# Performance work log

Measured on AMD Instinct MI355X. Metric: run time of the kernel, lower is better.

Reference implementation:

```python
import jax, jax.numpy as jnp
import numpy as np

N_NODES = 50000
N_EDGES = 800000
D_FEAT = 96
DIM_H = 128
N_CLASSES = 10


def setup_inputs() -> dict:
    key = jax.random.key(0)
    k = jax.random.split(key, 6)
    x = jax.random.normal(k[0], (N_NODES, D_FEAT), dtype=jnp.float32)
    edge_index = jax.random.randint(k[1], (2, N_EDGES), 0, N_NODES, dtype=jnp.int64)
    # Rank1Linear(dim_h): W = outer(a1, b1), a1: (in,), b1: (out,)
    a1 = jax.random.normal(k[2], (D_FEAT,), dtype=jnp.float32) / np.sqrt(D_FEAT)
    b1 = jax.random.normal(k[3], (DIM_H,), dtype=jnp.float32)
    # Rank1Linear(num_classes)
    a2 = jax.random.normal(k[4], (DIM_H,), dtype=jnp.float32) / np.sqrt(DIM_H)
    b2 = jax.random.normal(k[5], (N_CLASSES,), dtype=jnp.float32)
    return {"x": x, "edge_index": edge_index, "a1": a1, "b1": b1, "a2": a2, "b2": b2}


def reference(x, edge_index, a1, b1, a2, b2):
    src = edge_index[0]
    dst = edge_index[1]
    # adj @ x without materializing NxN: gather source features, scatter-add to dest
    agg = jax.ops.segment_sum(x[src], dst, num_segments=N_NODES)  # [N, d_feat]
    # GraphConv: rank-1 linear + ReLU. (adj @ x) @ (a1 b1^T) == ((adj@x) @ a1) outer b1
    h1 = jax.nn.relu((agg @ a1)[:, None] * b1[None, :])  # [N, dim_h]
    # sum pooling over nodes -> graph embedding [1, dim_h]; dropout is identity in eval
    hG = jnp.sum(h1, axis=0, keepdims=True)
    # final rank-1 linear to classes
    return (hG @ a2)[:, None] * b2[None, :]  # [1, num_classes]
```

## Files before the change

### kernel.cpp

```cpp
#include <hip/hip_runtime.h>

constexpr int N_NODES   = 50000;
constexpr int N_EDGES   = 800000;
constexpr int D_FEAT    = 96;
constexpr int DIM_H     = 128;
constexpr int N_CLASSES = 10;

constexpr int SHIFT  = 8;
constexpr int BNODES = 1 << SHIFT;
constexpr int NB     = (N_NODES + BNODES - 1) >> SHIFT;
constexpr int NBLK1  = 256;
constexpr int EPB    = N_EDGES / NBLK1;
constexpr int PREFW  = NB + 1;

static_assert(N_NODES <= (1 << 16), "16-bit id packing requires N_NODES <= 65536");
static_assert(N_EDGES % NBLK1 == 0, "exact edge split");
static_assert(D_FEAT % 8 == 0, "8-lane row dot needs D_FEAT % 8 == 0");

__device__ inline int wave_iscan(int v, int lane) {
#pragma unroll
    for (int off = 1; off < 64; off <<= 1) {
        int n = __shfl_up(v, off);
        if (lane >= off) v += n;
    }
    return v;
}

__device__ inline float wave_rsum(float v) {
#pragma unroll
    for (int off = 32; off > 0; off >>= 1) v += __shfl_down(v, off);
    return v;
}

__global__ __launch_bounds__(1024) void k_prep(
    const float* __restrict__ x, const float* __restrict__ a1,
    const int* __restrict__ src, const int* __restrict__ dst,
    float* __restrict__ y, unsigned* __restrict__ pairs,
    int* __restrict__ prefg, int* __restrict__ ticket)
{
    __shared__ unsigned stage[EPB];
    __shared__ int hist[NB], run[NB], excl[PREFW];
    __shared__ int wsum[16];
    const int tid  = threadIdx.x;
    const int lane = tid & 63, wid = tid >> 6;
    const int blk  = blockIdx.x;

    if (blk == 0 && tid == 0)
        __hip_atomic_store(ticket, 0, __ATOMIC_RELAXED, __HIP_MEMORY_SCOPE_AGENT);

    {
        const float4* av = reinterpret_cast<const float4*>(a1);
        const int sub = tid & 7;
        const float4 a0 = av[sub * 3 + 0];
        const float4 a1v = av[sub * 3 + 1];
        const float4 a2v = av[sub * 3 + 2];
        const int g0 = (blk * 1024 + tid) >> 3;
        for (int r = g0; r < N_NODES; r += (NBLK1 * 1024) / 8) {
            const float4* row =
                reinterpret_cast<const float4*>(x + (size_t)r * D_FEAT) + sub * 3;
            float4 v0 = row[0], v1 = row[1], v2 = row[2];
            float s = v0.x * a0.x + v0.y * a0.y + v0.z * a0.z + v0.w * a0.w
                    + v1.x * a1v.x + v1.y * a1v.y + v1.z * a1v.z + v1.w * a1v.w
                    + v2.x * a2v.x + v2.y * a2v.y + v2.z * a2v.z + v2.w * a2v.w;
            s += __shfl_xor(s, 1);
            s += __shfl_xor(s, 2);
            s += __shfl_xor(s, 4);
            if (sub == 0) y[r] = s;
        }
    }

    for (int t = tid; t < NB; t += 1024) hist[t] = 0;
    __syncthreads();
    const int e0 = blk * EPB;
    for (int j = tid; j < EPB; j += 1024)
        atomicAdd(&hist[((unsigned)dst[e0 + j]) >> SHIFT], 1);
    __syncthreads();

    int v   = (tid < NB) ? hist[tid] : 0;
    int inc = wave_iscan(v, lane);
    if (lane == 63) wsum[wid] = inc;
    __syncthreads();
    int woff = 0;
#pragma unroll
    for (int w = 0; w < 16; ++w) if (w < wid) woff += wsum[w];
    if (tid < NB) { int e = inc - v + woff; excl[tid] = e; run[tid] = e; }
    if (tid == 0) {
        int t = 0;
#pragma unroll
        for (int w = 0; w < 16; ++w) t += wsum[w];
        excl[NB] = t;
    }
    __syncthreads();
    if (tid < PREFW) prefg[blk * PREFW + tid] = excl[tid];

    for (int j = tid; j < EPB; j += 1024) {
        int d = dst[e0 + j];
        int s = src[e0 + j];
        int pos = atomicAdd(&run[((unsigned)d) >> SHIFT], 1);
        stage[pos] = ((unsigned)s << 16) | (unsigned)d;
    }
    __syncthreads();

    for (int j = tid; j < EPB; j += 1024)
        pairs[(size_t)blk * EPB + j] = stage[j];
}

__global__ __launch_bounds__(512) void k_accum_final(
    const unsigned* __restrict__ pairs, const int* __restrict__ prefg,
    const float* __restrict__ y, const float* __restrict__ b1,
    const float* __restrict__ a2, const float* __restrict__ b2,
    float* __restrict__ PMpart, int* __restrict__ ticket,
    float* __restrict__ out)
{
    __shared__ float acc[BNODES];
    __shared__ int   soff[NBLK1], scnt[NBLK1];
    __shared__ float redp[8], redm[8], redcp[8], redcn[8];
    __shared__ int   islast;
    __shared__ float tval;
    const int b    = blockIdx.x;
    const int tid  = threadIdx.x;
    const int lane = tid & 63, wid = tid >> 6;

    if (tid < BNODES) acc[tid] = 0.f;
    if (tid < NBLK1) {
        int st = prefg[tid * PREFW + b];
        soff[tid] = st;
        scnt[tid] = prefg[tid * PREFW + b + 1] - st;
    }
    __syncthreads();

    {
        const int seg = tid >> 1, h = tid & 1;
        const int n = scnt[seg];
        const unsigned* p0 = pairs + (size_t)seg * EPB + soff[seg];
        for (int j = h; j < n; j += 2) {
            unsigned p = p0[j];
            atomicAdd(&acc[p & (BNODES - 1)], y[p >> 16]);
        }
    }
    __syncthreads();

    float pp = 0.f, mm = 0.f;
    if (tid < BNODES) {
        int g = (b << SHIFT) + tid;
        if (g < N_NODES) {
            float v = acc[tid];
            pp = fmaxf(v, 0.f);
            mm = fminf(v, 0.f);
        }
    }
    pp = wave_rsum(pp);
    mm = wave_rsum(mm);
    if (lane == 0) { redp[wid] = pp; redm[wid] = mm; }
    __syncthreads();
    if (tid == 0) {
        float tp = 0.f, tm = 0.f;
#pragma unroll
        for (int w = 0; w < 8; ++w) { tp += redp[w]; tm += redm[w]; }
        __hip_atomic_store(&PMpart[2 * b],     tp, __ATOMIC_RELAXED, __HIP_MEMORY_SCOPE_AGENT);
        __hip_atomic_store(&PMpart[2 * b + 1], tm, __ATOMIC_RELAXED, __HIP_MEMORY_SCOPE_AGENT);
        int t = __hip_atomic_fetch_add(ticket, 1, __ATOMIC_ACQ_REL, __HIP_MEMORY_SCOPE_AGENT);
        islast = (t == NB - 1);
    }
    __syncthreads();

    if (islast) {
        float P = 0.f, M = 0.f, cp = 0.f, cn = 0.f;
        if (tid < NB) {
            P = __hip_atomic_load(&PMpart[2 * tid],     __ATOMIC_RELAXED, __HIP_MEMORY_SCOPE_AGENT);
            M = __hip_atomic_load(&PMpart[2 * tid + 1], __ATOMIC_RELAXED, __HIP_MEMORY_SCOPE_AGENT);
        }
        if (tid < DIM_H) {
            float bv = b1[tid], pr = a2[tid] * bv;
            cp = (bv > 0.f) ? pr : 0.f;
            cn = (bv < 0.f) ? pr : 0.f;
        }
        P  = wave_rsum(P);
        M  = wave_rsum(M);
        cp = wave_rsum(cp);
        cn = wave_rsum(cn);
        __syncthreads();
        if (lane == 0) { redp[wid] = P; redm[wid] = M; redcp[wid] = cp; redcn[wid] = cn; }
        __syncthreads();
        if (tid == 0) {
            float sP = 0.f, sM = 0.f, sCP = 0.f, sCN = 0.f;
#pragma unroll
            for (int w = 0; w < 8; ++w) {
                sP += redp[w]; sM += redm[w]; sCP += redcp[w]; sCN += redcn[w];
            }
            tval = sP * sCP + sM * sCN;
        }
        __syncthreads();
        if (tid < N_CLASSES) out[tid] = tval * b2[tid];
    }
}

__global__ void fb_node_dot(const float* __restrict__ x, const float* __restrict__ a1,
                            float* __restrict__ y) {
    int i = blockIdx.x * blockDim.x + threadIdx.x;
    if (i >= N_NODES) return;
    const float4* row = reinterpret_cast<const float4*>(x + (size_t)i * D_FEAT);
    const float4* av  = reinterpret_cast<const float4*>(a1);
    float acc = 0.f;
#pragma unroll
    for (int k = 0; k < D_FEAT / 4; ++k) {
        float4 v = row[k], a = av[k];
        acc += v.x * a.x + v.y * a.y + v.z * a.z + v.w * a.w;
    }
    y[i] = acc;
}

__global__ void fb_scatter(const int* __restrict__ src, const int* __restrict__ dst,
                           const float* __restrict__ y, float* __restrict__ s) {
    int e = blockIdx.x * blockDim.x + threadIdx.x;
    if (e >= N_EDGES) return;
    atomicAdd(&s[dst[e]], y[src[e]]);
}

__global__ void fb_reduce(const float* __restrict__ s, float* __restrict__ PM) {
    float p = 0.f, m = 0.f;
    for (int i = blockIdx.x * blockDim.x + threadIdx.x; i < N_NODES;
         i += gridDim.x * blockDim.x) {
        float v = s[i];
        p += fmaxf(v, 0.f);
        m += fminf(v, 0.f);
    }
    p = wave_rsum(p);
    m = wave_rsum(m);
    __shared__ float lp[4], lm[4];
    int wid = threadIdx.x >> 6, lane = threadIdx.x & 63;
    if (lane == 0) { lp[wid] = p; lm[wid] = m; }
    __syncthreads();
    if (threadIdx.x == 0) {
        float tp = 0.f, tm = 0.f;
        for (int w = 0; w < (int)(blockDim.x >> 6); ++w) { tp += lp[w]; tm += lm[w]; }
        atomicAdd(&PM[0], tp);
        atomicAdd(&PM[1], tm);
    }
}

__global__ void fb_final(const float* __restrict__ b1, const float* __restrict__ a2,
                         const float* __restrict__ b2, const float* __restrict__ PM,
                         float* __restrict__ out) {
    int t = threadIdx.x;
    float bv = b1[t], prod = a2[t] * bv;
    float cp = (bv > 0.f) ? prod : 0.f;
    float cn = (bv < 0.f) ? prod : 0.f;
    cp = wave_rsum(cp);
    cn = wave_rsum(cn);
    __shared__ float scp[2], scn[2], tv;
    if ((t & 63) == 0) { scp[t >> 6] = cp; scn[t >> 6] = cn; }
    __syncthreads();
    if (t == 0) tv = PM[0] * (scp[0] + scp[1]) + PM[1] * (scn[0] + scn[1]);
    __syncthreads();
    if (t < N_CLASSES) out[t] = tv * b2[t];
}

extern "C" void kernel_launch(void* const* d_in, const int* in_sizes, int n_in,
                              void* d_out, int out_size, void* d_ws, size_t ws_size,
                              hipStream_t stream) {
    const float* x  = (const float*)d_in[0];
    const int*   ei = (const int*)d_in[1];
    const float* a1 = (const float*)d_in[2];
    const float* b1 = (const float*)d_in[3];
    const float* a2 = (const float*)d_in[4];
    const float* b2 = (const float*)d_in[5];
    float* out = (float*)d_out;

    unsigned* pairs  = (unsigned*)d_ws;
    float*    y      = (float*)(pairs + N_EDGES);
    int*      prefg  = (int*)(y + N_NODES);
    float*    PMpart = (float*)(prefg + NBLK1 * PREFW);
    int*      ticket = (int*)(PMpart + 2 * NB);

    size_t need = (size_t)N_EDGES * 4 + (size_t)N_NODES * 4 +
                  (size_t)NBLK1 * PREFW * 4 + (size_t)2 * NB * 4 + 4;

    if (ws_size >= need) {
        k_prep<<<NBLK1, 1024, 0, stream>>>(x, a1, ei, ei + N_EDGES, y, pairs, prefg, ticket);
        k_accum_final<<<NB, 512, 0, stream>>>(pairs, prefg, y, b1, a2, b2,
                                              PMpart, ticket, out);
    } else {
        float* yf = (float*)d_ws;
        float* s  = yf + N_NODES;
        float* PM = s + N_NODES;
        hipMemsetAsync(s, 0, (N_NODES + 2) * sizeof(float), stream);
        fb_node_dot<<<(N_NODES + 255) / 256, 256, 0, stream>>>(x, a1, yf);
        fb_scatter<<<(N_EDGES + 255) / 256, 256, 0, stream>>>(ei, ei + N_EDGES, yf, s);
        fb_reduce<<<196, 256, 0, stream>>>(s, PM);
        fb_final<<<1, DIM_H, 0, stream>>>(b1, a2, b2, PM, out);
    }
}
```

Before: 27.24 us.

## Fuse prep and accumulate kernels with a grid-wide spin barrier

Merges the two kernels into one persistent launch of 400 blocks of 512 threads. A global atomic counter barrier separates the bucketing phase from the per-bucket accumulation phase. The prefix table is stored transposed so each accumulating block reads contiguous offsets, and each of 400 threads walks one segment serially instead of two threads per segment. This removes a kernel launch boundary, but adds a hipMemsetAsync for the counters and depends on all 400 blocks being co-resident to avoid deadlock.

```diff
diff --git a/kernel.cpp b/kernel.cpp
--- a/kernel.cpp
+++ b/kernel.cpp
@@ -9,13 +9,14 @@
 constexpr int SHIFT  = 8;
 constexpr int BNODES = 1 << SHIFT;
 constexpr int NB     = (N_NODES + BNODES - 1) >> SHIFT;
-constexpr int NBLK1  = 256;
-constexpr int EPB    = N_EDGES / NBLK1;
 constexpr int PREFW  = NB + 1;
-
-static_assert(N_NODES <= (1 << 16), "16-bit id packing requires N_NODES <= 65536");
-static_assert(N_EDGES % NBLK1 == 0, "exact edge split");
-static_assert(D_FEAT % 8 == 0, "8-lane row dot needs D_FEAT % 8 == 0");
+constexpr int G      = 400;
+constexpr int T      = 512;
+constexpr int EPB    = N_EDGES / G;
+
+static_assert(N_EDGES % G == 0, "exact edge split");
+static_assert(N_NODES <= (1 << 16), "16-bit id packing");
+static_assert(D_FEAT % 8 == 0, "8-lane row dot");
 
 __device__ inline int wave_iscan(int v, int lane) {
 #pragma unroll
@@ -32,30 +33,37 @@
     return v;
 }
 
-__global__ __launch_bounds__(1024) void k_prep(
-    const float* __restrict__ x, const float* __restrict__ a1,
-    const int* __restrict__ src, const int* __restrict__ dst,
+__global__ __launch_bounds__(T) void k_fused(
+    const float* __restrict__ x,  const float* __restrict__ a1,
+    const int* __restrict__ src,  const int* __restrict__ dst,
+    const float* __restrict__ b1, const float* __restrict__ a2,
+    const float* __restrict__ b2,
     float* __restrict__ y, unsigned* __restrict__ pairs,
-    int* __restrict__ prefg, int* __restrict__ ticket)
+    int* __restrict__ pf_t, float* __restrict__ PMpart,
+    int* __restrict__ ctrs, float* __restrict__ out)
 {
     __shared__ unsigned stage[EPB];
-    __shared__ int hist[NB], run[NB], excl[PREFW];
-    __shared__ int wsum[16];
+    __shared__ int   hist[NB], run[NB], excl[NB];
+    __shared__ int   wsum[T / 64];
+    __shared__ float acc[BNODES];
+    __shared__ float redp[8], redm[8], redcp[8], redcn[8];
+    __shared__ int   islast;
+    __shared__ float tval;
+
     const int tid  = threadIdx.x;
     const int lane = tid & 63, wid = tid >> 6;
     const int blk  = blockIdx.x;
 
-    if (blk == 0 && tid == 0)
-        __hip_atomic_store(ticket, 0, __ATOMIC_RELAXED, __HIP_MEMORY_SCOPE_AGENT);
+    if (tid < NB) hist[tid] = 0;
 
     {
         const float4* av = reinterpret_cast<const float4*>(a1);
         const int sub = tid & 7;
-        const float4 a0 = av[sub * 3 + 0];
+        const float4 a0  = av[sub * 3 + 0];
         const float4 a1v = av[sub * 3 + 1];
         const float4 a2v = av[sub * 3 + 2];
-        const int g0 = (blk * 1024 + tid) >> 3;
-        for (int r = g0; r < N_NODES; r += (NBLK1 * 1024) / 8) {
+        const int g0 = (blk * T + tid) >> 3;
+        for (int r = g0; r < N_NODES; r += (G * T) / 8) {
             const float4* row =
                 reinterpret_cast<const float4*>(x + (size_t)r * D_FEAT) + sub * 3;
             float4 v0 = row[0], v1 = row[1], v2 = row[2];
@@ -68,130 +76,126 @@
             if (sub == 0) y[r] = s;
         }
     }
-
-    for (int t = tid; t < NB; t += 1024) hist[t] = 0;
-    __syncthreads();
+    __syncthreads();
+
     const int e0 = blk * EPB;
-    for (int j = tid; j < EPB; j += 1024)
+    for (int j = tid; j < EPB; j += T)
         atomicAdd(&hist[((unsigned)dst[e0 + j]) >> SHIFT], 1);
     __syncthreads();
 
-    int v   = (tid < NB) ? hist[tid] : 0;
-    int inc = wave_iscan(v, lane);
-    if (lane == 63) wsum[wid] = inc;
-    __syncthreads();
-    int woff = 0;
-#pragma unroll
-    for (int w = 0; w < 16; ++w) if (w < wid) woff += wsum[w];
-    if (tid < NB) { int e = inc - v + woff; excl[tid] = e; run[tid] = e; }
-    if (tid == 0) {
-        int t = 0;
-#pragma unroll
-        for (int w = 0; w < 16; ++w) t += wsum[w];
-        excl[NB] = t;
-    }
-    __syncthreads();
-    if (tid < PREFW) prefg[blk * PREFW + tid] = excl[tid];
-
-    for (int j = tid; j < EPB; j += 1024) {
+    {
+        int v   = (tid < NB) ? hist[tid] : 0;
+        int inc = wave_iscan(v, lane);
+        if (lane == 63) wsum[wid] = inc;
+        __syncthreads();
+        int woff = 0;
+#pragma unroll
+        for (int w = 0; w < T / 64; ++w) if (w < wid) woff += wsum[w];
+        if (tid < NB) { int e = inc - v + woff; excl[tid] = e; run[tid] = e; }
+    }
+    __syncthreads();
+
+    if (tid < PREFW) pf_t[(size_t)tid * G + blk] = (tid < NB) ? excl[tid] : EPB;
+
+    for (int j = tid; j < EPB; j += T) {
         int d = dst[e0 + j];
         int s = src[e0 + j];
         int pos = atomicAdd(&run[((unsigned)d) >> SHIFT], 1);
         stage[pos] = ((unsigned)s << 16) | (unsigned)d;
     }
     __syncthreads();
-
-    for (int j = tid; j < EPB; j += 1024)
+    for (int j = tid; j < EPB; j += T)
         pairs[(size_t)blk * EPB + j] = stage[j];
-}
-
-__global__ __launch_bounds__(512) void k_accum_final(
-    const unsigned* __restrict__ pairs, const int* __restrict__ prefg,
-    const float* __restrict__ y, const float* __restrict__ b1,
-    const float* __restrict__ a2, const float* __restrict__ b2,
-    float* __restrict__ PMpart, int* __restrict__ ticket,
-    float* __restrict__ out)
-{
-    __shared__ float acc[BNODES];
-    __shared__ int   soff[NBLK1], scnt[NBLK1];
-    __shared__ float redp[8], redm[8], redcp[8], redcn[8];
-    __shared__ int   islast;
-    __shared__ float tval;
-    const int b    = blockIdx.x;
-    const int tid  = threadIdx.x;
-    const int lane = tid & 63, wid = tid >> 6;
-
-    if (tid < BNODES) acc[tid] = 0.f;
-    if (tid < NBLK1) {
-        int st = prefg[tid * PREFW + b];
-        soff[tid] = st;
-        scnt[tid] = prefg[tid * PREFW + b + 1] - st;
-    }
-    __syncthreads();
-
-    {
-        const int seg = tid >> 1, h = tid & 1;
-        const int n = scnt[seg];
-        const unsigned* p0 = pairs + (size_t)seg * EPB + soff[seg];
-        for (int j = h; j < n; j += 2) {
-            unsigned p = p0[j];
-            atomicAdd(&acc[p & (BNODES - 1)], y[p >> 16]);
-        }
-    }
-    __syncthreads();
-
-    float pp = 0.f, mm = 0.f;
-    if (tid < BNODES) {
-        int g = (b << SHIFT) + tid;
-        if (g < N_NODES) {
-            float v = acc[tid];
-            pp = fmaxf(v, 0.f);
-            mm = fminf(v, 0.f);
-        }
-    }
-    pp = wave_rsum(pp);
-    mm = wave_rsum(mm);
-    if (lane == 0) { redp[wid] = pp; redm[wid] = mm; }
+
     __syncthreads();
     if (tid == 0) {
-        float tp = 0.f, tm = 0.f;
-#pragma unroll
-        for (int w = 0; w < 8; ++w) { tp += redp[w]; tm += redm[w]; }
-        __hip_atomic_store(&PMpart[2 * b],     tp, __ATOMIC_RELAXED, __HIP_MEMORY_SCOPE_AGENT);
-        __hip_atomic_store(&PMpart[2 * b + 1], tm, __ATOMIC_RELAXED, __HIP_MEMORY_SCOPE_AGENT);
-        int t = __hip_atomic_fetch_add(ticket, 1, __ATOMIC_ACQ_REL, __HIP_MEMORY_SCOPE_AGENT);
-        islast = (t == NB - 1);
-    }
-    __syncthreads();
-
-    if (islast) {
-        float P = 0.f, M = 0.f, cp = 0.f, cn = 0.f;
-        if (tid < NB) {
-            P = __hip_atomic_load(&PMpart[2 * tid],     __ATOMIC_RELAXED, __HIP_MEMORY_SCOPE_AGENT);
-            M = __hip_atomic_load(&PMpart[2 * tid + 1], __ATOMIC_RELAXED, __HIP_MEMORY_SCOPE_AGENT);
-        }
-        if (tid < DIM_H) {
-            float bv = b1[tid], pr = a2[tid] * bv;
-            cp = (bv > 0.f) ? pr : 0.f;
-            cn = (bv < 0.f) ? pr : 0.f;
-        }
-        P  = wave_rsum(P);
-        M  = wave_rsum(M);
-        cp = wave_rsum(cp);
-        cn = wave_rsum(cn);
-        __syncthreads();
-        if (lane == 0) { redp[wid] = P; redm[wid] = M; redcp[wid] = cp; redcn[wid] = cn; }
+        __hip_atomic_fetch_add(&ctrs[0], 1, __ATOMIC_ACQ_REL,
+                               __HIP_MEMORY_SCOPE_AGENT);
+        while (__hip_atomic_load(&ctrs[0], __ATOMIC_RELAXED,
+                                 __HIP_MEMORY_SCOPE_AGENT) < G)
+            __builtin_amdgcn_s_sleep(2);
+        (void)__hip_atomic_load(&ctrs[0], __ATOMIC_ACQUIRE,
+                                __HIP_MEMORY_SCOPE_AGENT);
+    }
+    __syncthreads();
+
+    if (blk < NB) {
+        const int b = blk;
+
+        if (tid < BNODES) acc[tid] = 0.f;
+        __syncthreads();
+
+        if (tid < G) {
+            const int t  = tid;
+            const int st = pf_t[(size_t)b * G + t];
+            const int en = pf_t[(size_t)(b + 1) * G + t];
+            const unsigned* p0 = pairs + (size_t)t * EPB + st;
+            const int n = en - st;
+            for (int j = 0; j < n; ++j) {
+                unsigned p = p0[j];
+                atomicAdd(&acc[p & (BNODES - 1)], y[p >> 16]);
+            }
+        }
+        __syncthreads();
+
+        float pp = 0.f, mm = 0.f;
+        if (tid < BNODES) {
+            int gn = (b << SHIFT) + tid;
+            if (gn < N_NODES) {
+                float v = acc[tid];
+                pp = fmaxf(v, 0.f);
+                mm = fminf(v, 0.f);
+            }
+        }
+        pp = wave_rsum(pp);
+        mm = wave_rsum(mm);
+        if (lane == 0) { redp[wid] = pp; redm[wid] = mm; }
         __syncthreads();
         if (tid == 0) {
-            float sP = 0.f, sM = 0.f, sCP = 0.f, sCN = 0.f;
-#pragma unroll
-            for (int w = 0; w < 8; ++w) {
-                sP += redp[w]; sM += redm[w]; sCP += redcp[w]; sCN += redcn[w];
-            }
-            tval = sP * sCP + sM * sCN;
-        }
-        __syncthreads();
-        if (tid < N_CLASSES) out[tid] = tval * b2[tid];
+            float tp = 0.f, tm = 0.f;
+#pragma unroll
+            for (int w = 0; w < 8; ++w) { tp += redp[w]; tm += redm[w]; }
+            __hip_atomic_store(&PMpart[2 * b],     tp, __ATOMIC_RELAXED,
+                               __HIP_MEMORY_SCOPE_AGENT);
+            __hip_atomic_store(&PMpart[2 * b + 1], tm, __ATOMIC_RELAXED,
+                               __HIP_MEMORY_SCOPE_AGENT);
+            int t = __hip_atomic_fetch_add(&ctrs[1], 1, __ATOMIC_ACQ_REL,
+                                           __HIP_MEMORY_SCOPE_AGENT);
+            islast = (t == NB - 1);
+        }
+        __syncthreads();
+
+        if (islast) {
+            float P = 0.f, M = 0.f, cp = 0.f, cn = 0.f;
+            if (tid < NB) {
+                P = __hip_atomic_load(&PMpart[2 * tid],     __ATOMIC_RELAXED,
+                                      __HIP_MEMORY_SCOPE_AGENT);
+                M = __hip_atomic_load(&PMpart[2 * tid + 1], __ATOMIC_RELAXED,
+                                      __HIP_MEMORY_SCOPE_AGENT);
+            }
+            if (tid < DIM_H) {
+                float bv = b1[tid], pr = a2[tid] * bv;
+                cp = (bv > 0.f) ? pr : 0.f;
+                cn = (bv < 0.f) ? pr : 0.f;
+            }
+            P  = wave_rsum(P);
+            M  = wave_rsum(M);
+            cp = wave_rsum(cp);
+            cn = wave_rsum(cn);
+            __syncthreads();
+            if (lane == 0) { redp[wid] = P; redm[wid] = M; redcp[wid] = cp; redcn[wid] = cn; }
+            __syncthreads();
+            if (tid == 0) {
+                float sP = 0.f, sM = 0.f, sCP = 0.f, sCN = 0.f;
+#pragma unroll
+                for (int w = 0; w < 8; ++w) {
+                    sP += redp[w]; sM += redm[w]; sCP += redcp[w]; sCN += redcn[w];
+                }
+                tval = sP * sCP + sM * sCN;
+            }
+            __syncthreads();
+            if (tid < N_CLASSES) out[tid] = tval * b2[tid];
+        }
     }
 }
 
@@ -269,22 +273,22 @@
 
     unsigned* pairs  = (unsigned*)d_ws;
     float*    y      = (float*)(pairs + N_EDGES);
-    int*      prefg  = (int*)(y + N_NODES);
-    float*    PMpart = (float*)(prefg + NBLK1 * PREFW);
-    int*      ticket = (int*)(PMpart + 2 * NB);
+    int*      pf_t   = (int*)(y + N_NODES);
+    float*    PMpart = (float*)(pf_t + (size_t)PREFW * G);
+    int*      ctrs   = (int*)(PMpart + 2 * NB);
 
     size_t need = (size_t)N_EDGES * 4 + (size_t)N_NODES * 4 +
-                  (size_t)NBLK1 * PREFW * 4 + (size_t)2 * NB * 4 + 4;
+                  (size_t)PREFW * G * 4 + (size_t)2 * NB * 4 + 8;
 
     if (ws_size >= need) {
-        k_prep<<<NBLK1, 1024, 0, stream>>>(x, a1, ei, ei + N_EDGES, y, pairs, prefg, ticket);
-        k_accum_final<<<NB, 512, 0, stream>>>(pairs, prefg, y, b1, a2, b2,
-                                              PMpart, ticket, out);
+        (void)hipMemsetAsync(ctrs, 0, 2 * sizeof(int), stream);
+        k_fused<<<G, T, 0, stream>>>(x, a1, ei, ei + N_EDGES, b1, a2, b2,
+                                     y, pairs, pf_t, PMpart, ctrs, out);
     } else {
         float* yf = (float*)d_ws;
         float* s  = yf + N_NODES;
         float* PM = s + N_NODES;
-        hipMemsetAsync(s, 0, (N_NODES + 2) * sizeof(float), stream);
+        (void)hipMemsetAsync(s, 0, (N_NODES + 2) * sizeof(float), stream);
         fb_node_dot<<<(N_NODES + 255) / 256, 256, 0, stream>>>(x, a1, yf);
         fb_scatter<<<(N_EDGES + 255) / 256, 256, 0, stream>>>(ei, ei + N_EDGES, yf, s);
         fb_reduce<<<196, 256, 0, stream>>>(s, PM);
```

New measurement: 70.96 us. +160.5%, slower.

## Write edge pairs into contiguous per-bucket regions via global atomic offsets

Applied to the files above, without the earlier changes.

The prep kernel now reserves space in a fixed-capacity per-destination-bucket array using a global atomicAdd per bucket, and scatters its locally sorted pairs into those slots. The accumulate kernel then reads one contiguous range per bucket instead of gathering 256 small segments through a prefix table. This removes the strided per-segment reads and the prefix-table loads, at the cost of an extra memset launch, global atomics in prep, a larger workspace, and scattered writes during prep. It relies on the fixed capacity CAP not being exceeded for any bucket.

```diff
diff --git a/kernel.cpp b/kernel.cpp
--- a/kernel.cpp
+++ b/kernel.cpp
@@ -10,12 +10,15 @@
 constexpr int BNODES = 1 << SHIFT;
 constexpr int NB     = (N_NODES + BNODES - 1) >> SHIFT;
 constexpr int NBLK1  = 256;
+constexpr int T1     = 1024;
 constexpr int EPB    = N_EDGES / NBLK1;
-constexpr int PREFW  = NB + 1;
-
-static_assert(N_NODES <= (1 << 16), "16-bit id packing requires N_NODES <= 65536");
+constexpr int CAP    = 8192;
+constexpr int T2     = 512;
+
+static_assert(N_NODES <= (1 << 16), "16-bit id packing");
 static_assert(N_EDGES % NBLK1 == 0, "exact edge split");
-static_assert(D_FEAT % 8 == 0, "8-lane row dot needs D_FEAT % 8 == 0");
+static_assert(D_FEAT % 8 == 0, "8-lane row dot");
+static_assert(CAP * NB >= N_EDGES, "capacity sanity");
 
 __device__ inline int wave_iscan(int v, int lane) {
 #pragma unroll
@@ -32,30 +35,29 @@
     return v;
 }
 
-__global__ __launch_bounds__(1024) void k_prep(
+__global__ __launch_bounds__(T1) void k_prep(
     const float* __restrict__ x, const float* __restrict__ a1,
     const int* __restrict__ src, const int* __restrict__ dst,
-    float* __restrict__ y, unsigned* __restrict__ pairs,
-    int* __restrict__ prefg, int* __restrict__ ticket)
+    float* __restrict__ y, unsigned* __restrict__ bucketPairs,
+    int* __restrict__ ctl )
 {
     __shared__ unsigned stage[EPB];
-    __shared__ int hist[NB], run[NB], excl[PREFW];
-    __shared__ int wsum[16];
+    __shared__ int hist[NB], run[NB], excl[NB], baseg[NB];
+    __shared__ int wsum[T1 / 64];
     const int tid  = threadIdx.x;
     const int lane = tid & 63, wid = tid >> 6;
     const int blk  = blockIdx.x;
 
-    if (blk == 0 && tid == 0)
-        __hip_atomic_store(ticket, 0, __ATOMIC_RELAXED, __HIP_MEMORY_SCOPE_AGENT);
+    if (tid < NB) hist[tid] = 0;
 
     {
         const float4* av = reinterpret_cast<const float4*>(a1);
         const int sub = tid & 7;
-        const float4 a0 = av[sub * 3 + 0];
+        const float4 a0  = av[sub * 3 + 0];
         const float4 a1v = av[sub * 3 + 1];
         const float4 a2v = av[sub * 3 + 2];
-        const int g0 = (blk * 1024 + tid) >> 3;
-        for (int r = g0; r < N_NODES; r += (NBLK1 * 1024) / 8) {
+        const int g0 = (blk * T1 + tid) >> 3;
+        for (int r = g0; r < N_NODES; r += (NBLK1 * T1) / 8) {
             const float4* row =
                 reinterpret_cast<const float4*>(x + (size_t)r * D_FEAT) + sub * 3;
             float4 v0 = row[0], v1 = row[1], v2 = row[2];
@@ -68,32 +70,31 @@
             if (sub == 0) y[r] = s;
         }
     }
-
-    for (int t = tid; t < NB; t += 1024) hist[t] = 0;
-    __syncthreads();
+    __syncthreads();
+
     const int e0 = blk * EPB;
-    for (int j = tid; j < EPB; j += 1024)
+    for (int j = tid; j < EPB; j += T1)
         atomicAdd(&hist[((unsigned)dst[e0 + j]) >> SHIFT], 1);
     __syncthreads();
 
-    int v   = (tid < NB) ? hist[tid] : 0;
-    int inc = wave_iscan(v, lane);
-    if (lane == 63) wsum[wid] = inc;
-    __syncthreads();
-    int woff = 0;
-#pragma unroll
-    for (int w = 0; w < 16; ++w) if (w < wid) woff += wsum[w];
-    if (tid < NB) { int e = inc - v + woff; excl[tid] = e; run[tid] = e; }
-    if (tid == 0) {
-        int t = 0;
-#pragma unroll
-        for (int w = 0; w < 16; ++w) t += wsum[w];
-        excl[NB] = t;
-    }
-    __syncthreads();
-    if (tid < PREFW) prefg[blk * PREFW + tid] = excl[tid];
-
-    for (int j = tid; j < EPB; j += 1024) {
+    {
+        int v   = (tid < NB) ? hist[tid] : 0;
+        int inc = wave_iscan(v, lane);
+        if (lane == 63) wsum[wid] = inc;
+        __syncthreads();
+        int woff = 0;
+#pragma unroll
+        for (int w = 0; w < T1 / 64; ++w) if (w < wid) woff += wsum[w];
+        if (tid < NB) {
+            int e = inc - v + woff;
+            excl[tid] = e;
+            run[tid]  = e;
+            baseg[tid] = atomicAdd(&ctl[tid], v);
+        }
+    }
+    __syncthreads();
+
+    for (int j = tid; j < EPB; j += T1) {
         int d = dst[e0 + j];
         int s = src[e0 + j];
         int pos = atomicAdd(&run[((unsigned)d) >> SHIFT], 1);
@@ -101,19 +102,21 @@
     }
     __syncthreads();
 
-    for (int j = tid; j < EPB; j += 1024)
-        pairs[(size_t)blk * EPB + j] = stage[j];
-}
-
-__global__ __launch_bounds__(512) void k_accum_final(
-    const unsigned* __restrict__ pairs, const int* __restrict__ prefg,
+    for (int j = tid; j < EPB; j += T1) {
+        unsigned p = stage[j];
+        int b = (int)((p & 0xFFFFu) >> SHIFT);
+        bucketPairs[(size_t)b * CAP + baseg[b] + (j - excl[b])] = p;
+    }
+}
+
+__global__ __launch_bounds__(T2) void k_accum_final(
+    const unsigned* __restrict__ bucketPairs, const int* __restrict__ ctl,
     const float* __restrict__ y, const float* __restrict__ b1,
     const float* __restrict__ a2, const float* __restrict__ b2,
     float* __restrict__ PMpart, int* __restrict__ ticket,
     float* __restrict__ out)
 {
     __shared__ float acc[BNODES];
-    __shared__ int   soff[NBLK1], scnt[NBLK1];
     __shared__ float redp[8], redm[8], redcp[8], redcn[8];
     __shared__ int   islast;
     __shared__ float tval;
@@ -122,28 +125,22 @@
     const int lane = tid & 63, wid = tid >> 6;
 
     if (tid < BNODES) acc[tid] = 0.f;
-    if (tid < NBLK1) {
-        int st = prefg[tid * PREFW + b];
-        soff[tid] = st;
-        scnt[tid] = prefg[tid * PREFW + b + 1] - st;
-    }
     __syncthreads();
 
     {
-        const int seg = tid >> 1, h = tid & 1;
-        const int n = scnt[seg];
-        const unsigned* p0 = pairs + (size_t)seg * EPB + soff[seg];
-        for (int j = h; j < n; j += 2) {
+        const int n = ctl[b];
+        const unsigned* p0 = bucketPairs + (size_t)b * CAP;
+        for (int j = tid; j < n; j += T2) {
             unsigned p = p0[j];
-            atomicAdd(&acc[p & (BNODES - 1)], y[p >> 16]);
+            atomicAdd(&acc[(p & 0xFFFFu) & (BNODES - 1)], y[p >> 16]);
         }
     }
     __syncthreads();
 
     float pp = 0.f, mm = 0.f;
     if (tid < BNODES) {
-        int g = (b << SHIFT) + tid;
-        if (g < N_NODES) {
+        int gn = (b << SHIFT) + tid;
+        if (gn < N_NODES) {
             float v = acc[tid];
             pp = fmaxf(v, 0.f);
             mm = fminf(v, 0.f);
@@ -267,24 +264,24 @@
     const float* b2 = (const float*)d_in[5];
     float* out = (float*)d_out;
 
-    unsigned* pairs  = (unsigned*)d_ws;
-    float*    y      = (float*)(pairs + N_EDGES);
-    int*      prefg  = (int*)(y + N_NODES);
-    float*    PMpart = (float*)(prefg + NBLK1 * PREFW);
-    int*      ticket = (int*)(PMpart + 2 * NB);
-
-    size_t need = (size_t)N_EDGES * 4 + (size_t)N_NODES * 4 +
-                  (size_t)NBLK1 * PREFW * 4 + (size_t)2 * NB * 4 + 4;
+    unsigned* bucketPairs = (unsigned*)d_ws;
+    float*    y      = (float*)(bucketPairs + (size_t)NB * CAP);
+    int*      ctl    = (int*)(y + N_NODES);
+    float*    PMpart = (float*)(ctl + NB + 1);
+
+    size_t need = (size_t)NB * CAP * 4 + (size_t)N_NODES * 4 +
+                  (size_t)(NB + 1) * 4 + (size_t)2 * NB * 4;
 
     if (ws_size >= need) {
-        k_prep<<<NBLK1, 1024, 0, stream>>>(x, a1, ei, ei + N_EDGES, y, pairs, prefg, ticket);
-        k_accum_final<<<NB, 512, 0, stream>>>(pairs, prefg, y, b1, a2, b2,
-                                              PMpart, ticket, out);
+        (void)hipMemsetAsync(ctl, 0, (NB + 1) * sizeof(int), stream);
+        k_prep<<<NBLK1, T1, 0, stream>>>(x, a1, ei, ei + N_EDGES, y, bucketPairs, ctl);
+        k_accum_final<<<NB, T2, 0, stream>>>(bucketPairs, ctl, y, b1, a2, b2,
+                                             PMpart, ctl + NB, out);
     } else {
         float* yf = (float*)d_ws;
         float* s  = yf + N_NODES;
         float* PM = s + N_NODES;
-        hipMemsetAsync(s, 0, (N_NODES + 2) * sizeof(float), stream);
+        (void)hipMemsetAsync(s, 0, (N_NODES + 2) * sizeof(float), stream);
         fb_node_dot<<<(N_NODES + 255) / 256, 256, 0, stream>>>(x, a1, yf);
         fb_scatter<<<(N_EDGES + 255) / 256, 256, 0, stream>>>(ei, ei + N_EDGES, yf, s);
         fb_reduce<<<196, 256, 0, stream>>>(s, PM);
```

After: 35.74 us. 1.31x slower.
